# Optimization experiments

Measured on AMD Instinct MI355X. Metric: run time of the kernel, lower is better.

Reference implementation:

```python
import jax, jax.numpy as jnp
import numpy as np

START_TAG = 7
STOP_TAG = 8
NEG = -10000.0  # matches torch.full((1,K), -10000.) in the original


def setup_inputs() -> dict:
    key = jax.random.key(0)
    k1, k2, k3, k4 = jax.random.split(key, 4)
    B, T, K = 1024, 2048, 9  # K = output_dim + 2 (START/STOP hardcoded as 7/8)
    feats = jax.random.normal(k1, (B, T, K), dtype=jnp.float32)
    tags = jax.random.randint(k2, (B, T), 0, 7)            # valid labels 0..6
    lengths = jax.random.randint(k3, (B,), 1, T + 1)        # per-sentence lengths >= 1
    transitions = jax.random.normal(k4, (K, K), dtype=jnp.float32)
    transitions = transitions.at[START_TAG, :].set(NEG)     # never transition into START
    transitions = transitions.at[:, STOP_TAG].set(NEG)      # never transition out of STOP
    return {"feats": feats, "transitions": transitions, "tags": tags, "lengths": lengths}


def _crf_nll(feats, transitions, tags, lengths):
    # feats: [B,T,K] emissions, transitions[j,i] = score of i -> j
    B, T, K = feats.shape

    def fwd_one(feat, length):
        # CRF forward algorithm (log partition), vectorized over tags,
        # lax.scan over time; masked past `length` to emulate feats[:x_len].
        alpha0 = jnp.full((K,), NEG, feat.dtype).at[START_TAG].set(0.0)

        def step(alpha, inp):
            t, f = inp
            # alpha_new[j] = logsumexp_i(alpha[i] + transitions[j,i]) + feat[t,j]
            new = jax.nn.logsumexp(alpha[None, :] + transitions, axis=1) + f
            return jnp.where(t < length, new, alpha), None

        alpha, _ = jax.lax.scan(step, alpha0, (jnp.arange(T), feat))
        return jax.nn.logsumexp(alpha + transitions[STOP_TAG])

    fwd_scores = jax.vmap(fwd_one)(feats, lengths)  # [B]

    def gold_one(feat, tg, length):
        # _score_sentence: sum_t trans[tags[t], tags[t-1]] + feat[t, tags[t]]
        prev = jnp.concatenate([jnp.array([START_TAG], tg.dtype), tg[:-1]])
        step_scores = transitions[tg, prev] + jnp.take_along_axis(feat, tg[:, None], axis=1)[:, 0]
        mask = jnp.arange(tg.shape[0]) < length
        last = tg[length - 1]
        return jnp.sum(jnp.where(mask, step_scores, 0.0)) + transitions[STOP_TAG, last]

    gold_scores = jax.vmap(gold_one)(feats, tags, lengths)  # [B]

    # neg_log_likelihood accumulates (forward - gold) per sentence, then / n
    return jnp.mean(fwd_scores - gold_scores)


def reference(feats, transitions, tags, lengths):
    return _crf_nll(feats, transitions, tags, lengths)
```

## Files before the change

### kernel.cpp

```cpp
#include <hip/hip_runtime.h>


#define START_TAG 7
#define STOP_TAG  8
#define KDIM      9
#define NS        7
#define CPS       64
#define SLICES    8
#define NEGINF    (-1e30f)

__device__ __forceinline__ float rfl(float x) {
    return __int_as_float(__builtin_amdgcn_readfirstlane(__float_as_int(x)));
}

__global__ __launch_bounds__(256, 4) void crf_chunk_kernel(
    const float* __restrict__ feats,
    const float* __restrict__ trans,
    const int*   __restrict__ tags,
    const int*   __restrict__ lengths,
    float* __restrict__ g_seg,
    float* __restrict__ g_gold,
    int B, int T)
{
    __shared__ float s_trans[81];
    __shared__ float s_E[49];
    __shared__ float s_M[4 * 512];

    const int tid = threadIdx.x;
    if (tid < 81) s_trans[tid] = trans[tid];
    if (tid >= 128 && tid < 177) {
        int k = tid - 128;
        s_E[k] = __expf(trans[(k / 7) * 9 + (k % 7)]);
    }
    __syncthreads();

    const int widx = tid >> 6;
    const int W    = blockIdx.x * 4 + widx;
    const int s    = W / B;
    const int b    = W - s * B;

    const int    len   = lengths[b];
    const int*   tg    = tags  + (size_t)b * T;
    const float* fbase = feats + (size_t)b * T * KDIM;
    const int    Lb    = (len > 1) ? ((len - 1 + CPS - 1) / CPS) : 1;

    {
        const int gs = (s == 0) ? 0 : 1 + s * 8 * Lb;
        const int ge = (s == SLICES - 1) ? len : min(1 + (s + 1) * 8 * Lb, len);
        float g = 0.f;
        if (gs < ge) {
            int span = ge - gs;
            int per  = (span + 63) >> 6;
            int t0   = gs + (tid & 63) * per;
            if (t0 < ge) {
                int te   = min(t0 + per, ge);
                int prev = (t0 == 0) ? START_TAG : tg[t0 - 1];
                for (int k = 0; k < per; ++k) {
                    int t   = t0 + k;
                    int tc  = min(t, te - 1);
                    int cur = tg[tc];
                    float v = s_trans[cur * 9 + prev] + fbase[(size_t)tc * KDIM + cur];
                    g += (t < te) ? v : 0.f;
                    prev = cur;
                }
                if (len - 1 >= t0 && len - 1 < t0 + per && len - 1 < ge)
                    g += s_trans[STOP_TAG * 9 + tg[len - 1]];
            }
        }
        #pragma unroll
        for (int off = 32; off > 0; off >>= 1) g += __shfl_xor(g, off, 64);
        if ((tid & 63) == 0) g_gold[b * SLICES + s] = g;
    }

    {
        const int lane8  = tid & 7;
        const int k      = (tid >> 3) & 7;
        const int c      = s * 8 + k;
        const int tstart = 1 + c * Lb;
        const int tend   = min(tstart + Lb, len);

        if (lane8 < NS) {
            float* Mw = s_M + widx * 512 + k * 64;
            if (tstart < tend) {
                float E[49];
                #pragma unroll
                for (int e = 0; e < 49; ++e) E[e] = rfl(s_E[e]);

                int baddr[NS];
                #pragma unroll
                for (int j = 0; j < NS; ++j) baddr[j] = (((tid & 56) | j) << 2);

                float p[NS];
                #pragma unroll
                for (int j = 0; j < NS; ++j) p[j] = (j == lane8) ? 1.f : 0.f;
                float sc = 0.f;
                int rem = tend - tstart;

                const float* fp = fbase + (size_t)tstart * KDIM + lane8;

                #define CRF_MAT(EF) do {                                        \
                    float q[NS];                                                \
                    _Pragma("unroll")                                           \
                    for (int j = 0; j < NS; ++j) {                              \
                        float acc = E[j * 7] * p[0];                            \
                        _Pragma("unroll")                                       \
                        for (int i = 1; i < NS; ++i)                            \
                            acc = fmaf(E[j * 7 + i], p[i], acc);                \
                        q[j] = acc;                                             \
                    }                                                           \
                    _Pragma("unroll")                                           \
                    for (int j = 0; j < NS; ++j) p[j] = q[j] * EF[j];           \
                } while (0)

                #define CRF_BCAST(DST, XF) do {                                 \
                    float _e = __expf(XF);                                      \
                    _Pragma("unroll")                                           \
                    for (int j = 0; j < NS; ++j)                                \
                        DST[j] = __int_as_float(                                \
                            __builtin_amdgcn_ds_bpermute(                       \
                                baddr[j], __float_as_int(_e)));                 \
                } while (0)

                #define CRF_STEP(XF) do {                                       \
                    float _ef[NS];                                              \
                    CRF_BCAST(_ef, XF);                                         \
                    CRF_MAT(_ef);                                               \
                } while (0)

                #define CRF_RENORM() do {                                       \
                    float m = p[0];                                             \
                    _Pragma("unroll")                                           \
                    for (int j = 1; j < NS; ++j) m = fmaxf(m, p[j]);            \
                    float rm = __builtin_amdgcn_rcpf(m);                        \
                    _Pragma("unroll")                                           \
                    for (int j = 0; j < NS; ++j) p[j] *= rm;                    \
                    sc += __logf(m);                                            \
                } while (0)

                int o1 = KDIM * min(1, rem - 1);
                int o2 = KDIM * min(2, rem - 1);
                int o3 = KDIM * min(3, rem - 1);
                float x0 = fp[0], x1 = fp[o1], x2 = fp[o2], x3 = fp[o3];
                fp += 4 * KDIM;

                while (rem >= 8) {
                    float y0 = fp[0], y1 = fp[KDIM], y2 = fp[2 * KDIM], y3 = fp[3 * KDIM];
                    fp += 4 * KDIM;
                    float efA[NS], efB[NS], efC[NS], efD[NS];
                    CRF_BCAST(efA, x0);
                    CRF_BCAST(efB, x1);
                    CRF_BCAST(efC, x2);
                    CRF_BCAST(efD, x3);
                    CRF_MAT(efA); CRF_MAT(efB); CRF_MAT(efC); CRF_MAT(efD);
                    CRF_RENORM();
                    x0 = y0; x1 = y1; x2 = y2; x3 = y3;
                    rem -= 4;
                }
                if (rem > 4) {
                    int e1 = KDIM * min(1, rem - 5);
                    int e2 = KDIM * min(2, rem - 5);
                    float y0 = fp[0], y1 = fp[e1], y2 = fp[e2];
                    float efA[NS], efB[NS], efC[NS], efD[NS];
                    CRF_BCAST(efA, x0);
                    CRF_BCAST(efB, x1);
                    CRF_BCAST(efC, x2);
                    CRF_BCAST(efD, x3);
                    CRF_MAT(efA); CRF_MAT(efB); CRF_MAT(efC); CRF_MAT(efD);
                    CRF_RENORM();
                    x0 = y0; x1 = y1; x2 = y2;
                    rem -= 4;
                }
                CRF_STEP(x0);
                if (rem > 1) CRF_STEP(x1);
                if (rem > 2) CRF_STEP(x2);
                if (rem > 3) CRF_STEP(x3);

                #pragma unroll
                for (int j = 0; j < NS; ++j)
                    Mw[j * 8 + lane8] = __logf(p[j]) + sc;

                #undef CRF_MAT
                #undef CRF_BCAST
                #undef CRF_STEP
                #undef CRF_RENORM
            } else {
                #pragma unroll
                for (int j = 0; j < NS; ++j)
                    Mw[j * 8 + lane8] = (j == lane8) ? 0.f : NEGINF;
            }
        }
    }

    asm volatile("s_waitcnt lgkmcnt(0)" ::: "memory");

    {
        const int l  = tid & 63;
        const int i  = l & 7;
        float* sg = s_M + widx * 512;

        float A = sg[l];
        int baddr[NS];
        #pragma unroll
        for (int k = 0; k < NS; ++k) baddr[k] = ((k << 3) | i) << 2;

        #pragma unroll
        for (int c = 1; c < 8; ++c) {
            const float* Mr = sg + c * 64 + (l & 56);
            float4 r0 = *(const float4*)(Mr);
            float4 r1 = *(const float4*)(Mr + 4);
            float ac[NS];
            #pragma unroll
            for (int k = 0; k < NS; ++k)
                ac[k] = __int_as_float(__builtin_amdgcn_ds_bpermute(
                            baddr[k], __float_as_int(A)));
            float t0 = r0.x + ac[0], t1 = r0.y + ac[1], t2 = r0.z + ac[2];
            float t3 = r0.w + ac[3], t4 = r1.x + ac[4], t5 = r1.y + ac[5];
            float t6 = r1.z + ac[6];
            float tm = fmaxf(fmaxf(fmaxf(t0, t1), fmaxf(t2, t3)),
                             fmaxf(fmaxf(t4, t5), t6));
            float sum = ((__expf(t0 - tm) + __expf(t1 - tm)) +
                         (__expf(t2 - tm) + __expf(t3 - tm))) +
                        ((__expf(t4 - tm) + __expf(t5 - tm)) + __expf(t6 - tm));
            A = tm + __logf(sum);
        }
        g_seg[((size_t)(b * SLICES + s)) * 64 + l] = A;
    }
}

__global__ __launch_bounds__(64) void crf_fold_kernel(
    const float* __restrict__ feats,
    const float* __restrict__ trans,
    const float* __restrict__ g_seg,
    const float* __restrict__ g_gold,
    float* __restrict__ out,
    int B, int T)
{
    __shared__ float s_S[512];

    const int tid = threadIdx.x;
    const int b   = blockIdx.x;

    {
        const float* sp = g_seg + (size_t)b * 512;
        #pragma unroll
        for (int k = 0; k < 8; ++k) s_S[tid + 64 * k] = sp[tid + 64 * k];
    }
    float gg = (tid < 8) ? g_gold[b * SLICES + tid] : 0.f;
    gg += __shfl_xor(gg, 1, 8);
    gg += __shfl_xor(gg, 2, 8);
    gg += __shfl_xor(gg, 4, 8);
    __syncthreads();

    if (tid < 8) {
        const int  lane  = tid;
        const bool isrow = (lane < NS);
        const int  row   = isrow ? lane : 0;
        const float* fbase = feats + (size_t)b * T * KDIM;

        float a[NS];
        #pragma unroll
        for (int i = 0; i < NS; ++i)
            a[i] = trans[i * 9 + START_TAG] + fbase[i];
        float S;
        {
            float mm = fmaxf(fmaxf(fmaxf(a[0], a[1]), fmaxf(a[2], a[3])),
                             fmaxf(fmaxf(a[4], a[5]), a[6]));
            S = mm;
            #pragma unroll
            for (int i = 0; i < NS; ++i) a[i] -= mm;
        }

        const float* Mr0 = s_S + row * 8;
        float4 mA = *(const float4*)(Mr0);
        float4 mB = *(const float4*)(Mr0 + 4);
        #pragma unroll
        for (int w = 0; w < 8; ++w) {
            int wn = min(w + 1, 7);
            float4 nA = *(const float4*)(Mr0 + wn * 64);
            float4 nB = *(const float4*)(Mr0 + wn * 64 + 4);
            float t0 = mA.x + a[0], t1 = mA.y + a[1], t2 = mA.z + a[2];
            float t3 = mA.w + a[3], t4 = mB.x + a[4], t5 = mB.y + a[5];
            float t6 = mB.z + a[6];
            float tm = fmaxf(fmaxf(fmaxf(t0, t1), fmaxf(t2, t3)),
                             fmaxf(fmaxf(t4, t5), t6));
            float e0 = __expf(t0 - tm), e1 = __expf(t1 - tm), e2 = __expf(t2 - tm);
            float e3 = __expf(t3 - tm), e4 = __expf(t4 - tm), e5 = __expf(t5 - tm);
            float e6 = __expf(t6 - tm);
            float sum = ((e0 + e1) + (e2 + e3)) + ((e4 + e5) + e6);
            float na = isrow ? (tm + __logf(sum)) : NEGINF;
            float b0 = __shfl(na, 0, 8), b1 = __shfl(na, 1, 8), b2 = __shfl(na, 2, 8);
            float b3 = __shfl(na, 3, 8), b4 = __shfl(na, 4, 8), b5 = __shfl(na, 5, 8);
            float b6 = __shfl(na, 6, 8);
            float mm = fmaxf(fmaxf(fmaxf(b0, b1), fmaxf(b2, b3)),
                             fmaxf(fmaxf(b4, b5), b6));
            a[0] = b0 - mm; a[1] = b1 - mm; a[2] = b2 - mm;
            a[3] = b3 - mm; a[4] = b4 - mm; a[5] = b5 - mm;
            a[6] = b6 - mm;
            S += mm;
            mA = nA; mB = nB;
        }

        if (lane == 0) {
            float t0 = a[0] + trans[STOP_TAG * 9 + 0];
            float t1 = a[1] + trans[STOP_TAG * 9 + 1];
            float t2 = a[2] + trans[STOP_TAG * 9 + 2];
            float t3 = a[3] + trans[STOP_TAG * 9 + 3];
            float t4 = a[4] + trans[STOP_TAG * 9 + 4];
            float t5 = a[5] + trans[STOP_TAG * 9 + 5];
            float t6 = a[6] + trans[STOP_TAG * 9 + 6];
            float tm = fmaxf(fmaxf(fmaxf(t0, t1), fmaxf(t2, t3)),
                             fmaxf(fmaxf(t4, t5), t6));
            float sum = ((__expf(t0 - tm) + __expf(t1 - tm)) +
                         (__expf(t2 - tm) + __expf(t3 - tm))) +
                        ((__expf(t4 - tm) + __expf(t5 - tm)) + __expf(t6 - tm));
            float fwd = S + tm + __logf(sum);
            atomicAdd(out, (fwd - gg) * (1.0f / (float)B));
        }
    }
}

__global__ void init_out_kernel(float* out) {
    if (threadIdx.x == 0) out[0] = 0.f;
}

extern "C" void kernel_launch(void* const* d_in, const int* in_sizes, int n_in,
                              void* d_out, int out_size, void* d_ws, size_t ws_size,
                              hipStream_t stream) {
    const float* feats   = (const float*)d_in[0];
    const float* trans   = (const float*)d_in[1];
    const int*   tags    = (const int*)d_in[2];
    const int*   lengths = (const int*)d_in[3];

    int B = in_sizes[3];
    int T = in_sizes[2] / B;

    float* seg  = (float*)d_ws;
    float* gold = seg + (size_t)B * SLICES * 64;

    init_out_kernel<<<1, 64, 0, stream>>>((float*)d_out);
    crf_chunk_kernel<<<B * SLICES / 4, 256, 0, stream>>>(
        feats, trans, tags, lengths, seg, gold, B, T);
    crf_fold_kernel<<<B, 64, 0, stream>>>(
        feats, trans, seg, gold, (float*)d_out, B, T);
}
```

Measured before the change: 154.1 us.

## Double time chunks per sentence and load emissions directly instead of lane broadcast

Each sentence is now split into 128 time chunks over 16 slices instead of 64 over 8, which shortens the serial matrix-product chain each thread walks, and the fold kernel is widened to combine 16 slice matrices. Inside the chunk loop, each lane now loads all seven emission values per step itself and computes seven exps, replacing the per-lane exp plus ds_bpermute broadcast. Step batching drops from four to two per renormalisation. This trades more redundant global loads and exp work, more blocks, and a longer fold for shorter per-thread sequential dependency chains and no cross-lane shuffles.

```diff
diff --git a/kernel.cpp b/kernel.cpp
--- a/kernel.cpp
+++ b/kernel.cpp
@@ -5,8 +5,8 @@
 #define STOP_TAG  8
 #define KDIM      9
 #define NS        7
-#define CPS       64
-#define SLICES    8
+#define CPS       128
+#define SLICES    16
 #define NEGINF    (-1e30f)
 
 __device__ __forceinline__ float rfl(float x) {
@@ -86,19 +86,20 @@
                 #pragma unroll
                 for (int e = 0; e < 49; ++e) E[e] = rfl(s_E[e]);
 
-                int baddr[NS];
-                #pragma unroll
-                for (int j = 0; j < NS; ++j) baddr[j] = (((tid & 56) | j) << 2);
-
                 float p[NS];
                 #pragma unroll
                 for (int j = 0; j < NS; ++j) p[j] = (j == lane8) ? 1.f : 0.f;
-                float sc = 0.f;
-                int rem = tend - tstart;
-
-                const float* fp = fbase + (size_t)tstart * KDIM + lane8;
-
-                #define CRF_MAT(EF) do {                                        \
+                float sc  = 0.f;
+                int   rem = tend - tstart;
+
+                const float* fp = fbase + (size_t)tstart * KDIM;
+
+                #define L7(D, OFF) do {                                         \
+                    _Pragma("unroll")                                           \
+                    for (int i7 = 0; i7 < NS; ++i7) D[i7] = fp[(OFF) + i7];     \
+                } while (0)
+
+                #define CRF_STEP(X) do {                                        \
                     float q[NS];                                                \
                     _Pragma("unroll")                                           \
                     for (int j = 0; j < NS; ++j) {                              \
@@ -109,22 +110,7 @@
                         q[j] = acc;                                             \
                     }                                                           \
                     _Pragma("unroll")                                           \
-                    for (int j = 0; j < NS; ++j) p[j] = q[j] * EF[j];           \
-                } while (0)
-
-                #define CRF_BCAST(DST, XF) do {                                 \
-                    float _e = __expf(XF);                                      \
-                    _Pragma("unroll")                                           \
-                    for (int j = 0; j < NS; ++j)                                \
-                        DST[j] = __int_as_float(                                \
-                            __builtin_amdgcn_ds_bpermute(                       \
-                                baddr[j], __float_as_int(_e)));                 \
-                } while (0)
-
-                #define CRF_STEP(XF) do {                                       \
-                    float _ef[NS];                                              \
-                    CRF_BCAST(_ef, XF);                                         \
-                    CRF_MAT(_ef);                                               \
+                    for (int j = 0; j < NS; ++j) p[j] = q[j] * __expf(X[j]);    \
                 } while (0)
 
                 #define CRF_RENORM() do {                                       \
@@ -137,50 +123,38 @@
                     sc += __logf(m);                                            \
                 } while (0)
 
-                int o1 = KDIM * min(1, rem - 1);
-                int o2 = KDIM * min(2, rem - 1);
-                int o3 = KDIM * min(3, rem - 1);
-                float x0 = fp[0], x1 = fp[o1], x2 = fp[o2], x3 = fp[o3];
-                fp += 4 * KDIM;
-
-                while (rem >= 8) {
-                    float y0 = fp[0], y1 = fp[KDIM], y2 = fp[2 * KDIM], y3 = fp[3 * KDIM];
-                    fp += 4 * KDIM;
-                    float efA[NS], efB[NS], efC[NS], efD[NS];
-                    CRF_BCAST(efA, x0);
-                    CRF_BCAST(efB, x1);
-                    CRF_BCAST(efC, x2);
-                    CRF_BCAST(efD, x3);
-                    CRF_MAT(efA); CRF_MAT(efB); CRF_MAT(efC); CRF_MAT(efD);
+                float xa[NS], xb[NS];
+                L7(xa, 0);
+                {
+                    int o1 = (rem > 1) ? KDIM : 0;
+                    L7(xb, o1);
+                }
+
+                while (rem >= 4) {
+                    float ya[NS], yb[NS];
+                    L7(ya, 2 * KDIM);
+                    L7(yb, 3 * KDIM);
+                    CRF_STEP(xa);
+                    CRF_STEP(xb);
                     CRF_RENORM();
-                    x0 = y0; x1 = y1; x2 = y2; x3 = y3;
-                    rem -= 4;
+                    #pragma unroll
+                    for (int i = 0; i < NS; ++i) { xa[i] = ya[i]; xb[i] = yb[i]; }
+                    fp  += 2 * KDIM;
+                    rem -= 2;
                 }
-                if (rem > 4) {
-                    int e1 = KDIM * min(1, rem - 5);
-                    int e2 = KDIM * min(2, rem - 5);
-                    float y0 = fp[0], y1 = fp[e1], y2 = fp[e2];
-                    float efA[NS], efB[NS], efC[NS], efD[NS];
-                    CRF_BCAST(efA, x0);
-                    CRF_BCAST(efB, x1);
-                    CRF_BCAST(efC, x2);
-                    CRF_BCAST(efD, x3);
-                    CRF_MAT(efA); CRF_MAT(efB); CRF_MAT(efC); CRF_MAT(efD);
-                    CRF_RENORM();
-                    x0 = y0; x1 = y1; x2 = y2;
-                    rem -= 4;
+                CRF_STEP(xa);
+                if (rem > 1) CRF_STEP(xb);
+                if (rem > 2) {
+                    float yc[NS];
+                    L7(yc, 2 * KDIM);
+                    CRF_STEP(yc);
                 }
-                CRF_STEP(x0);
-                if (rem > 1) CRF_STEP(x1);
-                if (rem > 2) CRF_STEP(x2);
-                if (rem > 3) CRF_STEP(x3);
 
                 #pragma unroll
                 for (int j = 0; j < NS; ++j)
                     Mw[j * 8 + lane8] = __logf(p[j]) + sc;
 
-                #undef CRF_MAT
-                #undef CRF_BCAST
+                #undef L7
                 #undef CRF_STEP
                 #undef CRF_RENORM
             } else {
@@ -235,20 +209,21 @@
     float* __restrict__ out,
     int B, int T)
 {
-    __shared__ float s_S[512];
+    __shared__ float s_S[SLICES * 64];
 
     const int tid = threadIdx.x;
     const int b   = blockIdx.x;
 
     {
-        const float* sp = g_seg + (size_t)b * 512;
-        #pragma unroll
-        for (int k = 0; k < 8; ++k) s_S[tid + 64 * k] = sp[tid + 64 * k];
-    }
-    float gg = (tid < 8) ? g_gold[b * SLICES + tid] : 0.f;
-    gg += __shfl_xor(gg, 1, 8);
-    gg += __shfl_xor(gg, 2, 8);
-    gg += __shfl_xor(gg, 4, 8);
+        const float* sp = g_seg + (size_t)b * (SLICES * 64);
+        #pragma unroll
+        for (int k = 0; k < SLICES; ++k) s_S[tid + 64 * k] = sp[tid + 64 * k];
+    }
+    float gg = (tid < SLICES) ? g_gold[b * SLICES + tid] : 0.f;
+    gg += __shfl_xor(gg, 1, 16);
+    gg += __shfl_xor(gg, 2, 16);
+    gg += __shfl_xor(gg, 4, 16);
+    gg += __shfl_xor(gg, 8, 16);
     __syncthreads();
 
     if (tid < 8) {
@@ -274,8 +249,8 @@
         float4 mA = *(const float4*)(Mr0);
         float4 mB = *(const float4*)(Mr0 + 4);
         #pragma unroll
-        for (int w = 0; w < 8; ++w) {
-            int wn = min(w + 1, 7);
+        for (int w = 0; w < SLICES; ++w) {
+            int wn = min(w + 1, SLICES - 1);
             float4 nA = *(const float4*)(Mr0 + wn * 64);
             float4 nB = *(const float4*)(Mr0 + wn * 64 + 4);
             float t0 = mA.x + a[0], t1 = mA.y + a[1], t2 = mA.z + a[2];
```

Measured after the change: 164.6 us. 1.07x slower.
